# Performance work log

Measured on AMD Instinct MI355X. Metric: run time of the kernel, lower is better.

The kernel has to match this reference:

```python
import jax, jax.numpy as jnp
import numpy as np

DIM = 256
HEADS = 8
WS = 8
N = WS * WS  # 64 tokens per window


def _rel_pos_index(ws: int) -> np.ndarray:
    coords = np.arange(ws)
    grid = np.stack(np.meshgrid(coords, coords, indexing='ij')).reshape(2, -1)  # [2, ws^2]
    rel = grid[:, :, None] - grid[:, None, :]          # [2, N, N]
    rel = rel.transpose(1, 2, 0).copy()                # [N, N, 2]
    rel[:, :, 0] += ws - 1
    rel[:, :, 1] += ws - 1
    rel[:, :, 0] *= 2 * ws - 1
    return rel.sum(-1)                                 # [N, N] int

REL_IDX = jnp.asarray(_rel_pos_index(WS))


def setup_inputs() -> dict:
    key = jax.random.key(0)
    ks = jax.random.split(key, 9)
    B = 4096
    std = 0.02
    return {
        'query_tokens': jax.random.normal(ks[0], (B, N, DIM), jnp.float32),
        'source_tokens': jax.random.normal(ks[1], (B, N, DIM), jnp.float32),
        'Wq': jax.random.normal(ks[2], (DIM, DIM), jnp.float32) * std,
        'bq': jnp.zeros((DIM,), jnp.float32),
        'Wkv': jax.random.normal(ks[3], (DIM, 2 * DIM), jnp.float32) * std,
        'bkv': jnp.zeros((2 * DIM,), jnp.float32),
        'bias_table': jax.random.normal(ks[4], ((2 * WS - 1) ** 2, HEADS), jnp.float32) * std,
        'Wp': jax.random.normal(ks[5], (DIM, DIM), jnp.float32) * std,
        'bp': jnp.zeros((DIM,), jnp.float32),
    }


def reference(query_tokens, source_tokens, Wq, bq, Wkv, bkv, bias_table, Wp, bp):
    B_, n, C = query_tokens.shape
    d = C // HEADS
    scale = d ** -0.5
    # projections
    q = (query_tokens @ Wq + bq).reshape(B_, n, HEADS, d).transpose(0, 2, 1, 3) * scale  # [B,H,N,d]
    kv = (source_tokens @ Wkv + bkv).reshape(B_, n, 2, HEADS, d).transpose(2, 0, 3, 1, 4)
    k, v = kv[0], kv[1]                                    # [B,H,N,d]
    # attention with relative position bias
    attn = jnp.einsum('bhnd,bhmd->bhnm', q, k)             # [B,H,N,N]
    rel_bias = bias_table[REL_IDX]                         # [N,N,H]
    attn = attn + rel_bias.transpose(2, 0, 1)[None]        # + [1,H,N,N]
    attn = jax.nn.softmax(attn, axis=-1)
    out = jnp.einsum('bhnm,bhmd->bhnd', attn, v)           # [B,H,N,d]
    out = out.transpose(0, 2, 1, 3).reshape(B_, n, C)
    return out @ Wp + bp
```

## Files before the change

kernel.cpp:

```cpp
#include <hip/hip_runtime.h>

typedef __bf16 bf16;
typedef __bf16 bf16x8 __attribute__((ext_vector_type(8)));
typedef __bf16 bf16x4 __attribute__((ext_vector_type(4)));
typedef float  f32x4  __attribute__((ext_vector_type(4)));

#define LDA 264
#define LDS_ELEMS (2 * 64 * LDA)

static __device__ __forceinline__ f32x4 mfma16(bf16x8 a, bf16x8 b, f32x4 c) {
  return __builtin_amdgcn_mfma_f32_16x16x32_bf16(a, b, c, 0, 0, 0);
}

static __device__ __forceinline__ unsigned pk2(float x, float y) {
  union { bf16 h; unsigned short u; } a, b;
  a.h = (bf16)x; b.h = (bf16)y;
  return (unsigned)a.u | ((unsigned)b.u << 16);
}

static __device__ __forceinline__ bf16x8 redist(f32x4 t0, f32x4 t1,
                                                int srcA, bool hi) {
  unsigned p0 = pk2(t0[0], t0[1]);
  unsigned p1 = pk2(t0[2], t0[3]);
  unsigned p2 = pk2(t1[0], t1[1]);
  unsigned p3 = pk2(t1[2], t1[3]);
  int srcB = srcA + 16;
  unsigned a0 = __shfl(p0, srcA), a1 = __shfl(p1, srcA);
  unsigned a2 = __shfl(p2, srcA), a3 = __shfl(p3, srcA);
  unsigned b0 = __shfl(p0, srcB), b1 = __shfl(p1, srcB);
  unsigned b2 = __shfl(p2, srcB), b3 = __shfl(p3, srcB);
  union { unsigned u[4]; bf16x8 v; } r;
  r.u[0] = hi ? a2 : a0;
  r.u[1] = hi ? a3 : a1;
  r.u[2] = hi ? b2 : b0;
  r.u[3] = hi ? b3 : b1;
  return r.v;
}

__global__ void prep_kernel(const float* __restrict__ Wq, const float* __restrict__ Wkv,
                            const float* __restrict__ Wp, const float* __restrict__ btab,
                            bf16* __restrict__ WqT, bf16* __restrict__ WkvT,
                            bf16* __restrict__ WpT, float* __restrict__ biasT) {
  int idx = blockIdx.x * 512 + threadIdx.x;
  if (idx < 65536) {
    int n = idx >> 8, k = idx & 255;
    WqT[idx] = (bf16)(Wq[k * 256 + n] * 0.17677669529663687f);
  } else if (idx < 196608) {
    int j = idx - 65536, n = j >> 8, k = j & 255;
    WkvT[j] = (bf16)Wkv[k * 512 + n];
  } else if (idx < 262144) {
    int j = idx - 196608, n = j >> 8, k = j & 255;
    WpT[j] = (bf16)Wp[k * 256 + n];
  } else {
    int j = idx - 262144;
    int h = j >> 12, rq = (j >> 6) & 63, ck = j & 63;
    int rel = ((rq >> 3) - (ck >> 3) + 7) * 15 + ((rq & 7) - (ck & 7) + 7);
    biasT[j] = btab[rel * 8 + h];
  }
}

__global__ __launch_bounds__(512, 4) void fused_kernel(
    const float* __restrict__ Xq_g, const float* __restrict__ Xs_g,
    const float* __restrict__ bq,  const float* __restrict__ bkv,
    const float* __restrict__ bp,
    const bf16* __restrict__ WqT, const bf16* __restrict__ WkvT,
    const bf16* __restrict__ WpT, const float* __restrict__ biasT,
    float* __restrict__ out) {
  __shared__ __attribute__((aligned(16))) bf16 sm[LDS_ELEMS];
  const int tid  = (int)threadIdx.x;
  const int w    = tid >> 6;
  const int lane = tid & 63;
  const int c    = lane & 15;
  const int q    = lane >> 4;
  const int srcA = c + ((q & 1) << 5);
  const bool hi  = (q >> 1) != 0;
  bf16* X0 = sm;
  bf16* X1 = sm + 64 * LDA;
  const long long xoff = (long long)blockIdx.x * (64 * 256);

  {
    const float4* g0 = (const float4*)(Xs_g + xoff);
    const float4* g1 = (const float4*)(Xq_g + xoff);
    float4 v0[8], v1[8];
    #pragma unroll
    for (int i = 0; i < 8; ++i) v0[i] = g0[tid + i * 512];
    #pragma unroll
    for (int i = 0; i < 8; ++i) v1[i] = g1[tid + i * 512];
    #pragma unroll
    for (int i = 0; i < 8; ++i) {
      int chunk = tid + i * 512;
      int row = chunk >> 6, col = (chunk & 63) << 2;
      bf16x4 s0 = {(bf16)v0[i].x, (bf16)v0[i].y, (bf16)v0[i].z, (bf16)v0[i].w};
      bf16x4 s1 = {(bf16)v1[i].x, (bf16)v1[i].y, (bf16)v1[i].z, (bf16)v1[i].w};
      *(bf16x4*)(X0 + row * LDA + col) = s0;
      *(bf16x4*)(X1 + row * LDA + col) = s1;
    }
  }
  __syncthreads();

  bf16x8 ka[4];
  bf16x8 vb[2][2];
  bf16x8 qb[4];

  {
    f32x4 ak[2][4];
    f32x4 av[4][2];
    #pragma unroll
    for (int m = 0; m < 2; ++m) {
      f32x4 b4 = *(const f32x4*)(bkv + w * 32 + m * 16 + q * 4);
      #pragma unroll
      for (int n = 0; n < 4; ++n) ak[m][n] = b4;
    }
    #pragma unroll
    for (int n = 0; n < 2; ++n) {
      float bv = bkv[256 + w * 32 + n * 16 + c];
      #pragma unroll
      for (int m = 0; m < 4; ++m) av[m][n] = (f32x4){bv, bv, bv, bv};
    }
    #pragma unroll
    for (int kt = 0; kt < 8; ++kt) {
      bf16x8 xf[4], wk[2], wv[2];
      #pragma unroll
      for (int m = 0; m < 4; ++m)
        xf[m] = *(const bf16x8*)(X0 + (m * 16 + c) * LDA + kt * 32 + q * 8);
      #pragma unroll
      for (int m = 0; m < 2; ++m)
        wk[m] = *(const bf16x8*)(WkvT + (w * 32 + m * 16 + c) * 256 + kt * 32 + q * 8);
      #pragma unroll
      for (int n = 0; n < 2; ++n)
        wv[n] = *(const bf16x8*)(WkvT + (256 + w * 32 + n * 16 + c) * 256 + kt * 32 + q * 8);
      #pragma unroll
      for (int m = 0; m < 2; ++m)
        #pragma unroll
        for (int n = 0; n < 4; ++n)
          ak[m][n] = mfma16(wk[m], xf[n], ak[m][n]);
      #pragma unroll
      for (int m = 0; m < 4; ++m)
        #pragma unroll
        for (int n = 0; n < 2; ++n)
          av[m][n] = mfma16(xf[m], wv[n], av[m][n]);
    }
    #pragma unroll
    for (int t = 0; t < 4; ++t) ka[t] = redist(ak[0][t], ak[1][t], srcA, hi);
    #pragma unroll
    for (int n = 0; n < 2; ++n)
      #pragma unroll
      for (int t = 0; t < 2; ++t)
        vb[n][t] = redist(av[2 * t][n], av[2 * t + 1][n], srcA, hi);
  }

  {
    const float scale = 0.17677669529663687f;
    f32x4 aq[2][4];
    #pragma unroll
    for (int m = 0; m < 2; ++m) {
      f32x4 b4 = *(const f32x4*)(bq + w * 32 + m * 16 + q * 4);
      f32x4 s4 = {b4[0] * scale, b4[1] * scale, b4[2] * scale, b4[3] * scale};
      #pragma unroll
      for (int n = 0; n < 4; ++n) aq[m][n] = s4;
    }
    #pragma unroll
    for (int kt = 0; kt < 8; ++kt) {
      bf16x8 xf[4], wq[2];
      #pragma unroll
      for (int m = 0; m < 4; ++m)
        xf[m] = *(const bf16x8*)(X1 + (m * 16 + c) * LDA + kt * 32 + q * 8);
      #pragma unroll
      for (int m = 0; m < 2; ++m)
        wq[m] = *(const bf16x8*)(WqT + (w * 32 + m * 16 + c) * 256 + kt * 32 + q * 8);
      #pragma unroll
      for (int m = 0; m < 2; ++m)
        #pragma unroll
        for (int n = 0; n < 4; ++n)
          aq[m][n] = mfma16(wq[m], xf[n], aq[m][n]);
    }
    #pragma unroll
    for (int t = 0; t < 4; ++t) qb[t] = redist(aq[0][t], aq[1][t], srcA, hi);
  }
  __syncthreads();

  #pragma unroll
  for (int p = 0; p < 2; ++p) {
    f32x4 s[4][2];
    #pragma unroll
    for (int m = 0; m < 4; ++m)
      #pragma unroll
      for (int n = 0; n < 2; ++n)
        s[m][n] = *(const f32x4*)(biasT + w * 4096 +
                                  (p * 32 + n * 16 + c) * 64 + m * 16 + q * 4);
    #pragma unroll
    for (int m = 0; m < 4; ++m)
      #pragma unroll
      for (int n = 0; n < 2; ++n)
        s[m][n] = mfma16(ka[m], qb[p * 2 + n], s[m][n]);

    #pragma unroll
    for (int n = 0; n < 2; ++n) {
      float mx = s[0][n][0];
      #pragma unroll
      for (int m = 0; m < 4; ++m)
        #pragma unroll
        for (int r = 0; r < 4; ++r) mx = fmaxf(mx, s[m][n][r]);
      mx = fmaxf(mx, __shfl_xor(mx, 16));
      mx = fmaxf(mx, __shfl_xor(mx, 32));
      const float L2E = 1.4426950408889634f;
      float mb = mx * L2E;
      float sum = 0.f;
      #pragma unroll
      for (int m = 0; m < 4; ++m)
        #pragma unroll
        for (int r = 0; r < 4; ++r) {
          float t = exp2f(s[m][n][r] * L2E - mb);
          s[m][n][r] = t;
          sum += t;
        }
      sum += __shfl_xor(sum, 16);
      sum += __shfl_xor(sum, 32);
      float rl = __builtin_amdgcn_rcpf(sum);
      #pragma unroll
      for (int m = 0; m < 4; ++m)
        #pragma unroll
        for (int r = 0; r < 4; ++r) s[m][n][r] *= rl;
    }

    #pragma unroll
    for (int n = 0; n < 2; ++n) {
      bf16x8 pa0 = redist(s[0][n], s[1][n], srcA, hi);
      bf16x8 pa1 = redist(s[2][n], s[3][n], srcA, hi);
      #pragma unroll
      for (int d = 0; d < 2; ++d) {
        f32x4 o = (f32x4){0.f, 0.f, 0.f, 0.f};
        o = mfma16(pa0, vb[d][0], o);
        o = mfma16(pa1, vb[d][1], o);
        #pragma unroll
        for (int r = 0; r < 4; ++r)
          X0[(p * 32 + n * 16 + q * 4 + r) * LDA + w * 32 + d * 16 + c] = (bf16)o[r];
      }
    }
  }
  __syncthreads();

  {
    f32x4 acc[4][2];
    #pragma unroll
    for (int n = 0; n < 2; ++n) {
      float bv = bp[w * 32 + n * 16 + c];
      #pragma unroll
      for (int m = 0; m < 4; ++m) acc[m][n] = (f32x4){bv, bv, bv, bv};
    }
    #pragma unroll
    for (int kt = 0; kt < 8; ++kt) {
      bf16x8 af[4], bw[2];
      #pragma unroll
      for (int m = 0; m < 4; ++m)
        af[m] = *(const bf16x8*)(X0 + (m * 16 + c) * LDA + kt * 32 + q * 8);
      #pragma unroll
      for (int n = 0; n < 2; ++n)
        bw[n] = *(const bf16x8*)(WpT + (w * 32 + n * 16 + c) * 256 + kt * 32 + q * 8);
      #pragma unroll
      for (int m = 0; m < 4; ++m)
        #pragma unroll
        for (int n = 0; n < 2; ++n)
          acc[m][n] = mfma16(af[m], bw[n], acc[m][n]);
    }
    float* dst = out + xoff;
    #pragma unroll
    for (int m = 0; m < 4; ++m)
      #pragma unroll
      for (int n = 0; n < 2; ++n)
        #pragma unroll
        for (int r = 0; r < 4; ++r)
          dst[(m * 16 + q * 4 + r) * 256 + w * 32 + n * 16 + c] = acc[m][n][r];
  }
}

extern "C" void kernel_launch(void* const* d_in, const int* in_sizes, int n_in,
                              void* d_out, int out_size, void* d_ws, size_t ws_size,
                              hipStream_t stream) {
  const float* Xq   = (const float*)d_in[0];
  const float* Xs   = (const float*)d_in[1];
  const float* Wq   = (const float*)d_in[2];
  const float* bq   = (const float*)d_in[3];
  const float* Wkv  = (const float*)d_in[4];
  const float* bkv  = (const float*)d_in[5];
  const float* btab = (const float*)d_in[6];
  const float* Wp   = (const float*)d_in[7];
  const float* bp   = (const float*)d_in[8];
  float* out = (float*)d_out;

  char* ws = (char*)d_ws;
  bf16*  WqT   = (bf16*)(ws);
  bf16*  WkvT  = (bf16*)(ws + 131072);
  bf16*  WpT   = (bf16*)(ws + 393216);
  float* biasT = (float*)(ws + 524288);

  const int Bw = in_sizes[0] / (64 * 256);

  prep_kernel<<<dim3(576), dim3(512), 0, stream>>>(Wq, Wkv, Wp, btab,
                                                   WqT, WkvT, WpT, biasT);
  fused_kernel<<<dim3(Bw), dim3(512), 0, stream>>>(Xq, Xs, bq, bkv, bp,
                                                   WqT, WkvT, WpT, biasT, out);
}
```

Measured before the change: 842.7 us.

## Make fused kernel persistent over 8 windows with register-prefetched inputs

Each block now processes 8 consecutive windows in a loop. The next window's source and query tokens are loaded into registers while the current window computes, and the two LDS buffers alternate roles. The Q projection is split per half so fewer accumulators are live at once. The aim is to hide global-load latency and cut launch and block-startup cost. In exchange the grid is 8x smaller (512 blocks), which may underfill the CUs, and the prefetch registers raise register pressure. The code also assumes the batch is divisible by 8.

After: 1.796 ms. 113% more time.

```diff
diff --git a/kernel.cpp b/kernel.cpp
--- a/kernel.cpp
+++ b/kernel.cpp
@@ -7,6 +7,7 @@
 
 #define LDA 264
 #define LDS_ELEMS (2 * 64 * LDA)
+#define NWIN 8
 
 static __device__ __forceinline__ f32x4 mfma16(bf16x8 a, bf16x8 b, f32x4 c) {
   return __builtin_amdgcn_mfma_f32_16x16x32_bf16(a, b, c, 0, 0, 0);
@@ -35,6 +36,11 @@
   r.u[2] = hi ? b2 : b0;
   r.u[3] = hi ? b3 : b1;
   return r.v;
+}
+
+static __device__ __forceinline__ bf16x4 cvt4(float4 v) {
+  bf16x4 b = {(bf16)v.x, (bf16)v.y, (bf16)v.z, (bf16)v.w};
+  return b;
 }
 
 __global__ void prep_kernel(const float* __restrict__ Wq, const float* __restrict__ Wkv,
@@ -74,203 +80,248 @@
   const int q    = lane >> 4;
   const int srcA = c + ((q & 1) << 5);
   const bool hi  = (q >> 1) != 0;
-  bf16* X0 = sm;
-  bf16* X1 = sm + 64 * LDA;
-  const long long xoff = (long long)blockIdx.x * (64 * 256);
-
+  bf16* bufA = sm;
+  bf16* bufB = sm + 64 * LDA;
+  const int scol = lane << 2;
+  const long long base = (long long)blockIdx.x * NWIN;
+
+  bf16x4 qreg[8];
   {
-    const float4* g0 = (const float4*)(Xs_g + xoff);
-    const float4* g1 = (const float4*)(Xq_g + xoff);
-    float4 v0[8], v1[8];
-    #pragma unroll
-    for (int i = 0; i < 8; ++i) v0[i] = g0[tid + i * 512];
-    #pragma unroll
-    for (int i = 0; i < 8; ++i) v1[i] = g1[tid + i * 512];
-    #pragma unroll
-    for (int i = 0; i < 8; ++i) {
-      int chunk = tid + i * 512;
-      int row = chunk >> 6, col = (chunk & 63) << 2;
-      bf16x4 s0 = {(bf16)v0[i].x, (bf16)v0[i].y, (bf16)v0[i].z, (bf16)v0[i].w};
-      bf16x4 s1 = {(bf16)v1[i].x, (bf16)v1[i].y, (bf16)v1[i].z, (bf16)v1[i].w};
-      *(bf16x4*)(X0 + row * LDA + col) = s0;
-      *(bf16x4*)(X1 + row * LDA + col) = s1;
-    }
+    const float4* g0 = (const float4*)(Xs_g + base * 16384);
+    const float4* g1 = (const float4*)(Xq_g + base * 16384);
+    float4 sv0[8], qv0[8];
+    #pragma unroll
+    for (int j = 0; j < 8; ++j) sv0[j] = g0[tid + j * 512];
+    #pragma unroll
+    for (int j = 0; j < 8; ++j) qv0[j] = g1[tid + j * 512];
+    #pragma unroll
+    for (int j = 0; j < 8; ++j)
+      *(bf16x4*)(bufA + (w + 8 * j) * LDA + scol) = cvt4(sv0[j]);
+    #pragma unroll
+    for (int j = 0; j < 8; ++j) qreg[j] = cvt4(qv0[j]);
   }
-  __syncthreads();
 
   bf16x8 ka[4];
   bf16x8 vb[2][2];
-  bf16x8 qb[4];
-
-  {
-    f32x4 ak[2][4];
-    f32x4 av[4][2];
-    #pragma unroll
-    for (int m = 0; m < 2; ++m) {
-      f32x4 b4 = *(const f32x4*)(bkv + w * 32 + m * 16 + q * 4);
-      #pragma unroll
-      for (int n = 0; n < 4; ++n) ak[m][n] = b4;
-    }
-    #pragma unroll
-    for (int n = 0; n < 2; ++n) {
-      float bv = bkv[256 + w * 32 + n * 16 + c];
-      #pragma unroll
-      for (int m = 0; m < 4; ++m) av[m][n] = (f32x4){bv, bv, bv, bv};
-    }
-    #pragma unroll
-    for (int kt = 0; kt < 8; ++kt) {
-      bf16x8 xf[4], wk[2], wv[2];
+
+  #pragma unroll 2
+  for (int i = 0; i < NWIN; ++i) {
+    bf16* Xs_b = (i & 1) ? bufB : bufA;
+    bf16* Xq_b = (i & 1) ? bufA : bufB;
+    const long long win = base + i;
+
+    __syncthreads();
+    #pragma unroll
+    for (int j = 0; j < 8; ++j)
+      *(bf16x4*)(Xq_b + (w + 8 * j) * LDA + scol) = qreg[j];
+    float4 sv[8];
+    if (i < NWIN - 1) {
+      const float4* g0 = (const float4*)(Xs_g + (win + 1) * 16384);
+      #pragma unroll
+      for (int j = 0; j < 8; ++j) sv[j] = g0[tid + j * 512];
+    }
+    __syncthreads();
+
+    {
+      f32x4 ak[2][4];
+      #pragma unroll
+      for (int m = 0; m < 2; ++m) {
+        f32x4 b4 = *(const f32x4*)(bkv + w * 32 + m * 16 + q * 4);
+        #pragma unroll
+        for (int n = 0; n < 4; ++n) ak[m][n] = b4;
+      }
+      #pragma unroll
+      for (int kt = 0; kt < 8; ++kt) {
+        bf16x8 xf[4], wk[2];
+        #pragma unroll
+        for (int n = 0; n < 4; ++n)
+          xf[n] = *(const bf16x8*)(Xs_b + (n * 16 + c) * LDA + kt * 32 + q * 8);
+        #pragma unroll
+        for (int m = 0; m < 2; ++m)
+          wk[m] = *(const bf16x8*)(WkvT + (w * 32 + m * 16 + c) * 256 + kt * 32 + q * 8);
+        #pragma unroll
+        for (int m = 0; m < 2; ++m)
+          #pragma unroll
+          for (int n = 0; n < 4; ++n)
+            ak[m][n] = mfma16(wk[m], xf[n], ak[m][n]);
+      }
+      #pragma unroll
+      for (int t = 0; t < 4; ++t) ka[t] = redist(ak[0][t], ak[1][t], srcA, hi);
+    }
+    {
+      f32x4 av[4][2];
+      #pragma unroll
+      for (int n = 0; n < 2; ++n) {
+        float bv = bkv[256 + w * 32 + n * 16 + c];
+        #pragma unroll
+        for (int m = 0; m < 4; ++m) av[m][n] = (f32x4){bv, bv, bv, bv};
+      }
+      #pragma unroll
+      for (int kt = 0; kt < 8; ++kt) {
+        bf16x8 xf[4], wv[2];
+        #pragma unroll
+        for (int m = 0; m < 4; ++m)
+          xf[m] = *(const bf16x8*)(Xs_b + (m * 16 + c) * LDA + kt * 32 + q * 8);
+        #pragma unroll
+        for (int n = 0; n < 2; ++n)
+          wv[n] = *(const bf16x8*)(WkvT + (256 + w * 32 + n * 16 + c) * 256 + kt * 32 + q * 8);
+        #pragma unroll
+        for (int m = 0; m < 4; ++m)
+          #pragma unroll
+          for (int n = 0; n < 2; ++n)
+            av[m][n] = mfma16(xf[m], wv[n], av[m][n]);
+      }
+      #pragma unroll
+      for (int n = 0; n < 2; ++n)
+        #pragma unroll
+        for (int t = 0; t < 2; ++t)
+          vb[n][t] = redist(av[2 * t][n], av[2 * t + 1][n], srcA, hi);
+    }
+    bf16x4 srg[8];
+    if (i < NWIN - 1) {
+      #pragma unroll
+      for (int j = 0; j < 8; ++j) srg[j] = cvt4(sv[j]);
+    }
+    __syncthreads();
+
+    #pragma unroll
+    for (int p = 0; p < 2; ++p) {
+      f32x4 aq[2][2];
+      {
+        const float scale = 0.17677669529663687f;
+        #pragma unroll
+        for (int m = 0; m < 2; ++m) {
+          f32x4 b4 = *(const f32x4*)(bq + w * 32 + m * 16 + q * 4);
+          f32x4 s4 = {b4[0] * scale, b4[1] * scale, b4[2] * scale, b4[3] * scale};
+          aq[m][0] = s4; aq[m][1] = s4;
+        }
+      }
+      #pragma unroll
+      for (int kt = 0; kt < 8; ++kt) {
+        bf16x8 xf2[2], wq2[2];
+        #pragma unroll
+        for (int n = 0; n < 2; ++n)
+          xf2[n] = *(const bf16x8*)(Xq_b + ((p * 2 + n) * 16 + c) * LDA + kt * 32 + q * 8);
+        #pragma unroll
+        for (int m = 0; m < 2; ++m)
+          wq2[m] = *(const bf16x8*)(WqT + (w * 32 + m * 16 + c) * 256 + kt * 32 + q * 8);
+        #pragma unroll
+        for (int m = 0; m < 2; ++m)
+          #pragma unroll
+          for (int n = 0; n < 2; ++n)
+            aq[m][n] = mfma16(wq2[m], xf2[n], aq[m][n]);
+      }
+      bf16x8 qb0 = redist(aq[0][0], aq[1][0], srcA, hi);
+      bf16x8 qb1 = redist(aq[0][1], aq[1][1], srcA, hi);
+
+      f32x4 s[4][2];
       #pragma unroll
       for (int m = 0; m < 4; ++m)
-        xf[m] = *(const bf16x8*)(X0 + (m * 16 + c) * LDA + kt * 32 + q * 8);
-      #pragma unroll
-      for (int m = 0; m < 2; ++m)
-        wk[m] = *(const bf16x8*)(WkvT + (w * 32 + m * 16 + c) * 256 + kt * 32 + q * 8);
-      #pragma unroll
-      for (int n = 0; n < 2; ++n)
-        wv[n] = *(const bf16x8*)(WkvT + (256 + w * 32 + n * 16 + c) * 256 + kt * 32 + q * 8);
-      #pragma unroll
-      for (int m = 0; m < 2; ++m)
-        #pragma unroll
-        for (int n = 0; n < 4; ++n)
-          ak[m][n] = mfma16(wk[m], xf[n], ak[m][n]);
+        #pragma unroll
+        for (int n = 0; n < 2; ++n)
+          s[m][n] = *(const f32x4*)(biasT + w * 4096 +
+                                    (p * 32 + n * 16 + c) * 64 + m * 16 + q * 4);
+      #pragma unroll
+      for (int m = 0; m < 4; ++m) {
+        s[m][0] = mfma16(ka[m], qb0, s[m][0]);
+        s[m][1] = mfma16(ka[m], qb1, s[m][1]);
+      }
+
+      #pragma unroll
+      for (int n = 0; n < 2; ++n) {
+        float mx = s[0][n][0];
+        #pragma unroll
+        for (int m = 0; m < 4; ++m)
+          #pragma unroll
+          for (int r = 0; r < 4; ++r) mx = fmaxf(mx, s[m][n][r]);
+        mx = fmaxf(mx, __shfl_xor(mx, 16));
+        mx = fmaxf(mx, __shfl_xor(mx, 32));
+        const float L2E = 1.4426950408889634f;
+        float mb = mx * L2E;
+        float sum = 0.f;
+        #pragma unroll
+        for (int m = 0; m < 4; ++m)
+          #pragma unroll
+          for (int r = 0; r < 4; ++r) {
+            float t = exp2f(s[m][n][r] * L2E - mb);
+            s[m][n][r] = t;
+            sum += t;
+          }
+        sum += __shfl_xor(sum, 16);
+        sum += __shfl_xor(sum, 32);
+        float rl = __builtin_amdgcn_rcpf(sum);
+        #pragma unroll
+        for (int m = 0; m < 4; ++m)
+          #pragma unroll
+          for (int r = 0; r < 4; ++r) s[m][n][r] *= rl;
+      }
+
+      #pragma unroll
+      for (int n = 0; n < 2; ++n) {
+        bf16x8 pa0 = redist(s[0][n], s[1][n], srcA, hi);
+        bf16x8 pa1 = redist(s[2][n], s[3][n], srcA, hi);
+        #pragma unroll
+        for (int d = 0; d < 2; ++d) {
+          f32x4 o = (f32x4){0.f, 0.f, 0.f, 0.f};
+          o = mfma16(pa0, vb[d][0], o);
+          o = mfma16(pa1, vb[d][1], o);
+          #pragma unroll
+          for (int r = 0; r < 4; ++r)
+            Xs_b[(p * 32 + n * 16 + q * 4 + r) * LDA + w * 32 + d * 16 + c] = (bf16)o[r];
+        }
+      }
+    }
+    __syncthreads();
+
+    if (i < NWIN - 1) {
+      #pragma unroll
+      for (int j = 0; j < 8; ++j)
+        *(bf16x4*)(Xq_b + (w + 8 * j) * LDA + scol) = srg[j];
+    }
+    float4 qv[8];
+    if (i < NWIN - 1) {
+      const float4* g1 = (const float4*)(Xq_g + (win + 1) * 16384);
+      #pragma unroll
+      for (int j = 0; j < 8; ++j) qv[j] = g1[tid + j * 512];
+    }
+
+    {
+      f32x4 acc[4][2];
+      #pragma unroll
+      for (int n = 0; n < 2; ++n) {
+        float bv = bp[w * 32 + n * 16 + c];
+        #pragma unroll
+        for (int m = 0; m < 4; ++m) acc[m][n] = (f32x4){bv, bv, bv, bv};
+      }
+      #pragma unroll
+      for (int kt = 0; kt < 8; ++kt) {
+        bf16x8 af[4], bw[2];
+        #pragma unroll
+        for (int m = 0; m < 4; ++m)
+          af[m] = *(const bf16x8*)(Xs_b + (m * 16 + c) * LDA + kt * 32 + q * 8);
+        #pragma unroll
+        for (int n = 0; n < 2; ++n)
+          bw[n] = *(const bf16x8*)(WpT + (w * 32 + n * 16 + c) * 256 + kt * 32 + q * 8);
+        #pragma unroll
+        for (int m = 0; m < 4; ++m)
+          #pragma unroll
+          for (int n = 0; n < 2; ++n)
+            acc[m][n] = mfma16(af[m], bw[n], acc[m][n]);
+      }
+      float* dst = out + win * 16384;
       #pragma unroll
       for (int m = 0; m < 4; ++m)
         #pragma unroll
         for (int n = 0; n < 2; ++n)
-          av[m][n] = mfma16(xf[m], wv[n], av[m][n]);
-    }
-    #pragma unroll
-    for (int t = 0; t < 4; ++t) ka[t] = redist(ak[0][t], ak[1][t], srcA, hi);
-    #pragma unroll
-    for (int n = 0; n < 2; ++n)
-      #pragma unroll
-      for (int t = 0; t < 2; ++t)
-        vb[n][t] = redist(av[2 * t][n], av[2 * t + 1][n], srcA, hi);
-  }
-
-  {
-    const float scale = 0.17677669529663687f;
-    f32x4 aq[2][4];
-    #pragma unroll
-    for (int m = 0; m < 2; ++m) {
-      f32x4 b4 = *(const f32x4*)(bq + w * 32 + m * 16 + q * 4);
-      f32x4 s4 = {b4[0] * scale, b4[1] * scale, b4[2] * scale, b4[3] * scale};
-      #pragma unroll
-      for (int n = 0; n < 4; ++n) aq[m][n] = s4;
-    }
-    #pragma unroll
-    for (int kt = 0; kt < 8; ++kt) {
-      bf16x8 xf[4], wq[2];
-      #pragma unroll
-      for (int m = 0; m < 4; ++m)
-        xf[m] = *(const bf16x8*)(X1 + (m * 16 + c) * LDA + kt * 32 + q * 8);
-      #pragma unroll
-      for (int m = 0; m < 2; ++m)
-        wq[m] = *(const bf16x8*)(WqT + (w * 32 + m * 16 + c) * 256 + kt * 32 + q * 8);
-      #pragma unroll
-      for (int m = 0; m < 2; ++m)
-        #pragma unroll
-        for (int n = 0; n < 4; ++n)
-          aq[m][n] = mfma16(wq[m], xf[n], aq[m][n]);
-    }
-    #pragma unroll
-    for (int t = 0; t < 4; ++t) qb[t] = redist(aq[0][t], aq[1][t], srcA, hi);
-  }
-  __syncthreads();
-
-  #pragma unroll
-  for (int p = 0; p < 2; ++p) {
-    f32x4 s[4][2];
-    #pragma unroll
-    for (int m = 0; m < 4; ++m)
-      #pragma unroll
-      for (int n = 0; n < 2; ++n)
-        s[m][n] = *(const f32x4*)(biasT + w * 4096 +
-                                  (p * 32 + n * 16 + c) * 64 + m * 16 + q * 4);
-    #pragma unroll
-    for (int m = 0; m < 4; ++m)
-      #pragma unroll
-      for (int n = 0; n < 2; ++n)
-        s[m][n] = mfma16(ka[m], qb[p * 2 + n], s[m][n]);
-
-    #pragma unroll
-    for (int n = 0; n < 2; ++n) {
-      float mx = s[0][n][0];
-      #pragma unroll
-      for (int m = 0; m < 4; ++m)
-        #pragma unroll
-        for (int r = 0; r < 4; ++r) mx = fmaxf(mx, s[m][n][r]);
-      mx = fmaxf(mx, __shfl_xor(mx, 16));
-      mx = fmaxf(mx, __shfl_xor(mx, 32));
-      const float L2E = 1.4426950408889634f;
-      float mb = mx * L2E;
-      float sum = 0.f;
-      #pragma unroll
-      for (int m = 0; m < 4; ++m)
-        #pragma unroll
-        for (int r = 0; r < 4; ++r) {
-          float t = exp2f(s[m][n][r] * L2E - mb);
-          s[m][n][r] = t;
-          sum += t;
-        }
-      sum += __shfl_xor(sum, 16);
-      sum += __shfl_xor(sum, 32);
-      float rl = __builtin_amdgcn_rcpf(sum);
-      #pragma unroll
-      for (int m = 0; m < 4; ++m)
-        #pragma unroll
-        for (int r = 0; r < 4; ++r) s[m][n][r] *= rl;
-    }
-
-    #pragma unroll
-    for (int n = 0; n < 2; ++n) {
-      bf16x8 pa0 = redist(s[0][n], s[1][n], srcA, hi);
-      bf16x8 pa1 = redist(s[2][n], s[3][n], srcA, hi);
-      #pragma unroll
-      for (int d = 0; d < 2; ++d) {
-        f32x4 o = (f32x4){0.f, 0.f, 0.f, 0.f};
-        o = mfma16(pa0, vb[d][0], o);
-        o = mfma16(pa1, vb[d][1], o);
-        #pragma unroll
-        for (int r = 0; r < 4; ++r)
-          X0[(p * 32 + n * 16 + q * 4 + r) * LDA + w * 32 + d * 16 + c] = (bf16)o[r];
-      }
-    }
-  }
-  __syncthreads();
-
-  {
-    f32x4 acc[4][2];
-    #pragma unroll
-    for (int n = 0; n < 2; ++n) {
-      float bv = bp[w * 32 + n * 16 + c];
-      #pragma unroll
-      for (int m = 0; m < 4; ++m) acc[m][n] = (f32x4){bv, bv, bv, bv};
-    }
-    #pragma unroll
-    for (int kt = 0; kt < 8; ++kt) {
-      bf16x8 af[4], bw[2];
-      #pragma unroll
-      for (int m = 0; m < 4; ++m)
-        af[m] = *(const bf16x8*)(X0 + (m * 16 + c) * LDA + kt * 32 + q * 8);
-      #pragma unroll
-      for (int n = 0; n < 2; ++n)
-        bw[n] = *(const bf16x8*)(WpT + (w * 32 + n * 16 + c) * 256 + kt * 32 + q * 8);
-      #pragma unroll
-      for (int m = 0; m < 4; ++m)
-        #pragma unroll
-        for (int n = 0; n < 2; ++n)
-          acc[m][n] = mfma16(af[m], bw[n], acc[m][n]);
-    }
-    float* dst = out + xoff;
-    #pragma unroll
-    for (int m = 0; m < 4; ++m)
-      #pragma unroll
-      for (int n = 0; n < 2; ++n)
-        #pragma unroll
-        for (int r = 0; r < 4; ++r)
-          dst[(m * 16 + q * 4 + r) * 256 + w * 32 + n * 16 + c] = acc[m][n][r];
+          #pragma unroll
+          for (int r = 0; r < 4; ++r)
+            dst[(m * 16 + q * 4 + r) * 256 + w * 32 + n * 16 + c] = acc[m][n][r];
+    }
+
+    if (i < NWIN - 1) {
+      #pragma unroll
+      for (int j = 0; j < 8; ++j) qreg[j] = cvt4(qv[j]);
+    }
   }
 }
 
@@ -298,6 +349,6 @@
 
   prep_kernel<<<dim3(576), dim3(512), 0, stream>>>(Wq, Wkv, Wp, btab,
                                                    WqT, WkvT, WpT, biasT);
-  fused_kernel<<<dim3(Bw), dim3(512), 0, stream>>>(Xq, Xs, bq, bkv, bp,
-                                                   WqT, WkvT, WpT, biasT, out);
-}
+  fused_kernel<<<dim3(Bw / NWIN), dim3(512), 0, stream>>>(Xq, Xs, bq, bkv, bp,
+                                                          WqT, WkvT, WpT, biasT, out);
+}
```
